# Optimization experiments

Hardware: AMD Instinct MI355X
Metric: run time of the kernel (lower is better)

Reference implementation:

```python
import jax, jax.numpy as jnp
import numpy as np

B, T, C = 4, 2048, 1024


def setup_inputs() -> dict:
    key = jax.random.key(0)
    ks = jax.random.split(key, 5)
    s = 1.0 / np.sqrt(C)
    return {
        "X": jax.random.normal(ks[0], (B, T, C), dtype=jnp.float32),
        "Wq": jax.random.normal(ks[1], (C, C), dtype=jnp.float32) * s,
        "Wk": jax.random.normal(ks[2], (C, C), dtype=jnp.float32) * s,
        "Wv": jax.random.normal(ks[3], (C, C), dtype=jnp.float32) * s,
        "Wo": jax.random.normal(ks[4], (C, C), dtype=jnp.float32) * s,
    }


def reference(X, Wq, Wk, Wv, Wo):
    Bx, Tx, Cx = X.shape
    Q = X @ Wq  # [B,T,C]
    K = X @ Wk
    V = X @ Wv
    scores = jnp.einsum('btc,bsc->bts', Q, K) / jnp.sqrt(jnp.asarray(Cx, X.dtype))
    # causal mask: position t attends to s <= t
    causal = jnp.tril(jnp.ones((Tx, Tx), dtype=bool))
    scores = jnp.where(causal, scores, jnp.asarray(-jnp.inf, scores.dtype))
    weights = jax.nn.softmax(scores, axis=-1)
    out = jnp.einsum('bts,bsc->btc', weights, V)
    return out @ Wo
```

## Files before the change

kernel.cpp:

```cpp
#include <hip/hip_runtime.h>
#include <hip/hip_bf16.h>
#include <cmath>


typedef __attribute__((ext_vector_type(8))) __bf16 bf16x8;
typedef __attribute__((ext_vector_type(8))) short short8;
typedef __attribute__((ext_vector_type(4))) float f32x4;

__device__ __forceinline__ unsigned short f2bf(float f) {
  union { float f; unsigned u; } v; v.f = f;
  unsigned u = v.u;
  u += ((u >> 16) & 1u) + 0x7fffu;
  return (unsigned short)(u >> 16);
}
__device__ __forceinline__ float bf2f(unsigned short h) {
  union { unsigned u; float f; } v; v.u = ((unsigned)h) << 16;
  return v.f;
}

#define GLDS(gp, sp)                                                           \
  __builtin_amdgcn_global_load_lds(                                            \
      (const __attribute__((address_space(1))) void*)(gp),                     \
      (__attribute__((address_space(3))) void*)(sp), 16, 0, 0)

__global__ void prep(const float* __restrict__ X,
                     const float* __restrict__ w0, const float* __restrict__ w1,
                     const float* __restrict__ w2, const float* __restrict__ w3,
                     unsigned short* __restrict__ Xb,
                     unsigned short* __restrict__ wcat,
                     unsigned short* __restrict__ wot,
                     int n) {
  if (blockIdx.z < 4) {
    const float* src = blockIdx.z == 0 ? w0 : blockIdx.z == 1 ? w1
                       : blockIdx.z == 2 ? w2 : w3;
    unsigned short* dst =
        blockIdx.z < 3 ? wcat + (size_t)blockIdx.z * n * n : wot;
    __shared__ float tile[32][33];
    int bx = blockIdx.x * 32, by = blockIdx.y * 32;
    int tx = threadIdx.x, ty = threadIdx.y;
#pragma unroll
    for (int i = 0; i < 32; i += 8)
      tile[ty + i][tx] = src[(size_t)(by + ty + i) * n + bx + tx];
    __syncthreads();
#pragma unroll
    for (int i = 0; i < 32; i += 8)
      dst[(size_t)(bx + ty + i) * n + by + tx] = f2bf(tile[tx][ty + i]);
  } else {
    const int bid = (blockIdx.z - 4) * 1024 + blockIdx.y * 32 + blockIdx.x;
    const int t = threadIdx.y * 32 + threadIdx.x;
    const int i = (bid * 256 + t) * 4;
    float4 f = *(const float4*)(X + i);
    ushort4 o = make_ushort4(f2bf(f.x), f2bf(f.y), f2bf(f.z), f2bf(f.w));
    *(ushort4*)(Xb + i) = o;
  }
}

__global__ __launch_bounds__(256, 2)
void gemm_qkv(const unsigned short* __restrict__ A, int lda,
              const unsigned short* __restrict__ B, int ldb,
              unsigned short* __restrict__ Cp, int K, int gx) {
  const int id = blockIdx.x;
  const int gs = gx * 8;
  const int g = id / gs, r = id - g * gs;
  const int bx = r >> 3;
  const int by = g * 8 + (r & 7);
  const int m0 = by * 128;
  const int n0 = bx * 128;

  const int tid  = threadIdx.x;
  const int lane = tid & 63;
  const int w    = tid >> 6;
  const int wm   = (w >> 1) * 64;
  const int wn   = (w & 1) * 64;
  const int quad = lane >> 4;
  const int l16  = lane & 15;

  __shared__ unsigned short As[8192];
  __shared__ unsigned short Bs[8192];

  f32x4 acc[4][4];
#pragma unroll
  for (int i = 0; i < 4; ++i)
#pragma unroll
    for (int j = 0; j < 4; ++j)
      acc[i][j] = (f32x4){0.f, 0.f, 0.f, 0.f};

  const int srow = tid >> 3;
  const int scol = ((tid & 7) ^ (srow & 7)) * 8;
  const unsigned short* gA = A + (long long)(m0 + srow) * lda + scol;
  const unsigned short* gB = B + (long long)(n0 + srow) * ldb + scol;
  const int rsw = l16 & 7;

  for (int kt = 0; kt < K; kt += 64) {
    __syncthreads();
#pragma unroll
    for (int r2 = 0; r2 < 4; ++r2) {
      GLDS(gA + (long long)(r2 * 32) * lda + kt, As + r2 * 2048 + tid * 8);
      GLDS(gB + (long long)(r2 * 32) * ldb + kt, Bs + r2 * 2048 + tid * 8);
    }
    __syncthreads();
#pragma unroll
    for (int ks = 0; ks < 2; ++ks) {
      bf16x8 af[4], bfr[4];
#pragma unroll
      for (int i = 0; i < 4; ++i)
        af[i] = *(const bf16x8*)(As + (wm + i * 16 + l16) * 64 +
                                 ((ks * 4 + quad) ^ rsw) * 8);
#pragma unroll
      for (int j = 0; j < 4; ++j)
        bfr[j] = *(const bf16x8*)(Bs + (wn + j * 16 + l16) * 64 +
                                  ((ks * 4 + quad) ^ rsw) * 8);
#pragma unroll
      for (int i = 0; i < 4; ++i)
#pragma unroll
        for (int j = 0; j < 4; ++j)
          acc[i][j] = __builtin_amdgcn_mfma_f32_16x16x32_bf16(af[i], bfr[j],
                                                              acc[i][j], 0, 0, 0);
    }
  }

#pragma unroll
  for (int i = 0; i < 4; ++i) {
#pragma unroll
    for (int j = 0; j < 4; ++j) {
      const int row = m0 + wm + i * 16 + quad * 4;
      const int col = n0 + wn + j * 16 + l16;
      if (col >= 2048) {
        const int b = row >> 11, t = row & 2047, cv = col - 2048;
        ushort4 o = make_ushort4(f2bf(acc[i][j][0]), f2bf(acc[i][j][1]),
                                 f2bf(acc[i][j][2]), f2bf(acc[i][j][3]));
        *(ushort4*)(Cp + 16777216LL + ((long long)(b * 1024 + cv)) * 2048 + t) = o;
      } else {
        unsigned short* dst = Cp + (col >= 1024 ? 8388608LL - 1024 : 0);
#pragma unroll
        for (int r2 = 0; r2 < 4; ++r2)
          dst[(long long)(row + r2) * 1024 + col] = f2bf(acc[i][j][r2]);
      }
    }
  }
}

template <typename OutT>
__global__ __launch_bounds__(64, 2)
void gemm64(const unsigned short* __restrict__ A, int lda, long long sA,
            const unsigned short* __restrict__ B, int ldb, long long sB,
            OutT* __restrict__ Cp, int ldc, long long sC,
            int K, float alpha, int tri, int kcap) {
  A  += (long long)blockIdx.z * sA;
  B  += (long long)blockIdx.z * sB;
  Cp += (long long)blockIdx.z * sC;

  int by, bx;
  if (tri) {
    const int idx = blockIdx.x;
    by = (int)((sqrtf(8.f * idx + 1.f) - 1.f) * 0.5f);
    while (by * (by + 1) / 2 > idx) --by;
    while ((by + 1) * (by + 2) / 2 <= idx) ++by;
    bx = idx - by * (by + 1) / 2;
  } else {
    by = blockIdx.y;
    bx = blockIdx.x;
    if (kcap) by = gridDim.y - 1 - by;
  }
  const int m0 = by * 64;
  const int n0 = bx * 64;
  const int Keff = kcap ? min(K, m0 + 64) : K;

  const int lane = threadIdx.x;
  const int quad = lane >> 4;
  const int l16  = lane & 15;
  const int rsw  = l16 & 7;

  __shared__ unsigned short As[4096];
  __shared__ unsigned short Bs[4096];

  f32x4 acc[4][4];
#pragma unroll
  for (int i = 0; i < 4; ++i)
#pragma unroll
    for (int j = 0; j < 4; ++j)
      acc[i][j] = (f32x4){0.f, 0.f, 0.f, 0.f};

  const int srow = lane >> 3;
  const int scol = ((lane & 7) ^ (srow & 7)) * 8;
  const unsigned short* gA = A + (long long)(m0 + srow) * lda + scol;
  const unsigned short* gB = B + (long long)(n0 + srow) * ldb + scol;

  for (int kt = 0; kt < Keff; kt += 64) {
    __syncthreads();
#pragma unroll
    for (int r = 0; r < 8; ++r) {
      GLDS(gA + (long long)(r * 8) * lda + kt, As + r * 512 + lane * 8);
      GLDS(gB + (long long)(r * 8) * ldb + kt, Bs + r * 512 + lane * 8);
    }
    __syncthreads();
#pragma unroll
    for (int ks = 0; ks < 2; ++ks) {
      bf16x8 af[4], bfr[4];
#pragma unroll
      for (int i = 0; i < 4; ++i)
        af[i] = *(const bf16x8*)(As + (i * 16 + l16) * 64 +
                                 ((ks * 4 + quad) ^ rsw) * 8);
#pragma unroll
      for (int j = 0; j < 4; ++j)
        bfr[j] = *(const bf16x8*)(Bs + (j * 16 + l16) * 64 +
                                  ((ks * 4 + quad) ^ rsw) * 8);
#pragma unroll
      for (int i = 0; i < 4; ++i)
#pragma unroll
        for (int j = 0; j < 4; ++j)
          acc[i][j] = __builtin_amdgcn_mfma_f32_16x16x32_bf16(af[i], bfr[j],
                                                              acc[i][j], 0, 0, 0);
    }
  }

#pragma unroll
  for (int i = 0; i < 4; ++i) {
#pragma unroll
    for (int j = 0; j < 4; ++j) {
      const int row = m0 + i * 16 + quad * 4;
      const int col = n0 + j * 16 + l16;
#pragma unroll
      for (int r = 0; r < 4; ++r) {
        float v = acc[i][j][r] * alpha;
        if constexpr (sizeof(OutT) == 2)
          Cp[(long long)(row + r) * ldc + col] = (OutT)f2bf(v);
        else
          Cp[(long long)(row + r) * ldc + col] = v;
      }
    }
  }
}

__global__ __launch_bounds__(256)
void softmax_causal(unsigned short* __restrict__ S, int T) {
  const long long row = blockIdx.x;
  const int t = (int)(row & (long long)(T - 1));
  const int limit = ((t >> 6) + 1) << 6;
  unsigned short* p = S + row * T;
  const int tid  = threadIdx.x;
  const int base = tid * 8;
  const bool active = base < limit;

  short8 raw = {};
  if (active) raw = *(const short8*)(p + base);
  float x[8];
  float mx = -1e30f;
#pragma unroll
  for (int j = 0; j < 8; ++j) {
    bool valid = active && (base + j) <= t;
    x[j] = valid ? bf2f((unsigned short)raw[j]) : -1e30f;
    mx = fmaxf(mx, x[j]);
  }
#pragma unroll
  for (int off = 32; off > 0; off >>= 1) mx = fmaxf(mx, __shfl_xor(mx, off));
  __shared__ float red[8];
  const int wv = tid >> 6;
  if ((tid & 63) == 0) red[wv] = mx;
  __syncthreads();
  mx = fmaxf(fmaxf(red[0], red[1]), fmaxf(red[2], red[3]));

  float sum = 0.f;
#pragma unroll
  for (int j = 0; j < 8; ++j) {
    bool valid = active && (base + j) <= t;
    x[j] = valid ? __expf(x[j] - mx) : 0.f;
    sum += x[j];
  }
#pragma unroll
  for (int off = 32; off > 0; off >>= 1) sum += __shfl_xor(sum, off);
  if ((tid & 63) == 0) red[4 + wv] = sum;
  __syncthreads();
  sum = red[4] + red[5] + red[6] + red[7];
  const float inv = 1.f / sum;

  if (active) {
    unsigned short out[8];
#pragma unroll
    for (int j = 0; j < 8; ++j) out[j] = f2bf(x[j] * inv);
    *(short8*)(p + base) = *(const short8*)out;
  }
}

extern "C" void kernel_launch(void* const* d_in, const int* in_sizes, int n_in,
                              void* d_out, int out_size, void* d_ws,
                              size_t ws_size, hipStream_t stream) {
  (void)in_sizes; (void)n_in; (void)out_size; (void)ws_size;
  const int Bb = 4, T = 2048, C = 1024;
  const int M = Bb * T;

  const float* X  = (const float*)d_in[0];
  const float* Wq = (const float*)d_in[1];
  const float* Wk = (const float*)d_in[2];
  const float* Wv = (const float*)d_in[3];
  const float* Wo = (const float*)d_in[4];
  float* Out = (float*)d_out;

  char* w = (char*)d_ws;
  unsigned short* Xb   = (unsigned short*)w; w += (size_t)M * C * 2;
  unsigned short* Wcat = (unsigned short*)w; w += (size_t)3 * C * C * 2;
  unsigned short* Wot  = (unsigned short*)w; w += (size_t)C * C * 2;
  unsigned short* Q    = (unsigned short*)w; w += (size_t)M * C * 2;
  unsigned short* Kb   = (unsigned short*)w; w += (size_t)M * C * 2;
  unsigned short* Vt   = (unsigned short*)w; w += (size_t)M * C * 2;
  unsigned short* O    = Xb;
  unsigned short* S    = (unsigned short*)d_out;

  prep<<<dim3(32, 32, 12), dim3(32, 8), 0, stream>>>(X, Wq, Wk, Wv, Wo, Xb,
                                                     Wcat, Wot, C);

  gemm_qkv<<<dim3((3 * C / 128) * (M / 128)), dim3(256), 0, stream>>>(
      Xb, C, Wcat, C, Q, C, 3 * C / 128);

  const int ntri = (T / 64) * (T / 64 + 1) / 2;
  gemm64<unsigned short><<<dim3(ntri, 1, Bb), dim3(64), 0, stream>>>(
      Q, C, (long long)T * C, Kb, C, (long long)T * C,
      S, T, (long long)T * T, C, 0.03125f, 1, 0);

  softmax_causal<<<M, 256, 0, stream>>>(S, T);

  gemm64<unsigned short><<<dim3(C / 64, T / 64, Bb), dim3(64), 0, stream>>>(
      S, T, (long long)T * T, Vt, T, (long long)C * T,
      O, C, (long long)T * C, T, 1.f, 0, 1);

  gemm64<float><<<dim3(C / 64, M / 64, 1), dim3(64), 0, stream>>>(
      O, C, 0, Wot, C, 0, Out, C, 0, C, 1.f, 0, 0);
}
```

Baseline: 282.2 us.

## Fold output projection into V weights and widen attention GEMM tiles to 128

Precomputes Wv·Wo as a combined weight so the V projection directly yields V·Wo, which removes the final output-projection GEMM. The P·V GEMM now writes fp32 output into a scratch buffer that is then copied to the output. The attention GEMMs move from single-wave 64x64 tiles to 128x128 tiles with 4 or 8 waves, and the softmax row limit is rounded to 128-wide blocks to match. In exchange, the folded weight product adds bf16 rounding and the change adds a device-to-device copy.

```diff
diff --git a/kernel.cpp b/kernel.cpp
--- a/kernel.cpp
+++ b/kernel.cpp
@@ -28,13 +28,21 @@
                      const float* __restrict__ w2, const float* __restrict__ w3,
                      unsigned short* __restrict__ Xb,
                      unsigned short* __restrict__ wcat,
+                     unsigned short* __restrict__ wvb,
                      unsigned short* __restrict__ wot,
                      int n) {
-  if (blockIdx.z < 4) {
-    const float* src = blockIdx.z == 0 ? w0 : blockIdx.z == 1 ? w1
-                       : blockIdx.z == 2 ? w2 : w3;
-    unsigned short* dst =
-        blockIdx.z < 3 ? wcat + (size_t)blockIdx.z * n * n : wot;
+  if (blockIdx.z == 2) {
+    int bx = blockIdx.x * 32, by = blockIdx.y * 32;
+    int tx = threadIdx.x, ty = threadIdx.y;
+#pragma unroll
+    for (int i = 0; i < 32; i += 8) {
+      size_t idx = (size_t)(by + ty + i) * n + bx + tx;
+      wvb[idx] = f2bf(w2[idx]);
+    }
+  } else if (blockIdx.z < 4) {
+    const float* src = blockIdx.z == 0 ? w0 : blockIdx.z == 1 ? w1 : w3;
+    unsigned short* dst = blockIdx.z == 0 ? wcat
+                          : blockIdx.z == 1 ? wcat + (size_t)n * n : wot;
     __shared__ float tile[32][33];
     int bx = blockIdx.x * 32, by = blockIdx.y * 32;
     int tx = threadIdx.x, ty = threadIdx.y;
@@ -52,6 +60,110 @@
     float4 f = *(const float4*)(X + i);
     ushort4 o = make_ushort4(f2bf(f.x), f2bf(f.y), f2bf(f.z), f2bf(f.w));
     *(ushort4*)(Xb + i) = o;
+  }
+}
+
+template <typename OutT, int NW>
+__global__ __launch_bounds__(NW * 64, NW / 2)
+void gemm_bt(const unsigned short* __restrict__ A, int lda, long long sA,
+             const unsigned short* __restrict__ B, int ldb, long long sB,
+             OutT* __restrict__ Cp, int ldc, long long sC,
+             int K, float alpha, int tri, int kcap, int gx) {
+  A  += (long long)blockIdx.z * sA;
+  B  += (long long)blockIdx.z * sB;
+  Cp += (long long)blockIdx.z * sC;
+
+  int by, bx;
+  if (tri) {
+    const int idx = blockIdx.x;
+    by = (int)((sqrtf(8.f * idx + 1.f) - 1.f) * 0.5f);
+    while (by * (by + 1) / 2 > idx) --by;
+    while ((by + 1) * (by + 2) / 2 <= idx) ++by;
+    bx = idx - by * (by + 1) / 2;
+  } else if (gx > 0) {
+    const int id = blockIdx.x;
+    const int gs = gx * 8;
+    const int g = id / gs, r = id - g * gs;
+    bx = r >> 3;
+    by = g * 8 + (r & 7);
+    if (kcap) by = (gridDim.x / gx) - 1 - by;
+  } else {
+    by = blockIdx.y;
+    bx = blockIdx.x;
+  }
+  const int m0 = by * 128;
+  const int n0 = bx * 128;
+  const int Keff = kcap ? min(K, m0 + 128) : K;
+
+  const int tid  = threadIdx.x;
+  const int lane = tid & 63;
+  const int w    = tid >> 6;
+  const int wm   = (NW == 4) ? (w >> 1) * 64 : (w >> 1) * 32;
+  const int wn   = (w & 1) * 64;
+  const int quad = lane >> 4;
+  const int l16  = lane & 15;
+  constexpr int AI = (NW == 4) ? 4 : 2;
+  constexpr int NR = 128 / (NW * 8);
+
+  __shared__ unsigned short As[8192];
+  __shared__ unsigned short Bs[8192];
+
+  f32x4 acc[AI][4];
+#pragma unroll
+  for (int i = 0; i < AI; ++i)
+#pragma unroll
+    for (int j = 0; j < 4; ++j)
+      acc[i][j] = (f32x4){0.f, 0.f, 0.f, 0.f};
+
+  const int srow = tid >> 3;
+  const int scol = ((tid & 7) ^ (srow & 7)) * 8;
+  const unsigned short* gA = A + (long long)(m0 + srow) * lda + scol;
+  const unsigned short* gB = B + (long long)(n0 + srow) * ldb + scol;
+  const int rsw = l16 & 7;
+
+  for (int kt = 0; kt < Keff; kt += 64) {
+    __syncthreads();
+#pragma unroll
+    for (int r = 0; r < NR; ++r) {
+      GLDS(gA + (long long)(r * NW * 8) * lda + kt, As + r * NW * 512 + tid * 8);
+      GLDS(gB + (long long)(r * NW * 8) * ldb + kt, Bs + r * NW * 512 + tid * 8);
+    }
+    __syncthreads();
+#pragma unroll
+    for (int ks = 0; ks < 2; ++ks) {
+      bf16x8 af[AI], bfr[4];
+#pragma unroll
+      for (int i = 0; i < AI; ++i)
+        af[i] = *(const bf16x8*)(As + (wm + i * 16 + l16) * 64 +
+                                 ((ks * 4 + quad) ^ rsw) * 8);
+#pragma unroll
+      for (int j = 0; j < 4; ++j)
+        bfr[j] = *(const bf16x8*)(Bs + (wn + j * 16 + l16) * 64 +
+                                  ((ks * 4 + quad) ^ rsw) * 8);
+#pragma unroll
+      for (int i = 0; i < AI; ++i)
+#pragma unroll
+        for (int j = 0; j < 4; ++j)
+          acc[i][j] = __builtin_amdgcn_mfma_f32_16x16x32_bf16(af[i], bfr[j],
+                                                              acc[i][j], 0, 0, 0);
+    }
+  }
+
+#pragma unroll
+  for (int i = 0; i < AI; ++i) {
+#pragma unroll
+    for (int j = 0; j < 4; ++j) {
+      const int row = m0 + wm + i * 16 + quad * 4;
+      const int col = n0 + wn + j * 16 + l16;
+#pragma unroll
+      for (int r = 0; r < 4; ++r) {
+        float v = acc[i][j][r] * alpha;
+        if constexpr (sizeof(OutT) == 2)
+          Cp[(long long)(row + r) * ldc + col] = (OutT)f2bf(v);
+        else
+          Cp[(long long)(row + r) * ldc + col] = v;
+      }
+    }
   }
 }
 
@@ -140,103 +252,11 @@
   }
 }
 
-template <typename OutT>
-__global__ __launch_bounds__(64, 2)
-void gemm64(const unsigned short* __restrict__ A, int lda, long long sA,
-            const unsigned short* __restrict__ B, int ldb, long long sB,
-            OutT* __restrict__ Cp, int ldc, long long sC,
-            int K, float alpha, int tri, int kcap) {
-  A  += (long long)blockIdx.z * sA;
-  B  += (long long)blockIdx.z * sB;
-  Cp += (long long)blockIdx.z * sC;
-
-  int by, bx;
-  if (tri) {
-    const int idx = blockIdx.x;
-    by = (int)((sqrtf(8.f * idx + 1.f) - 1.f) * 0.5f);
-    while (by * (by + 1) / 2 > idx) --by;
-    while ((by + 1) * (by + 2) / 2 <= idx) ++by;
-    bx = idx - by * (by + 1) / 2;
-  } else {
-    by = blockIdx.y;
-    bx = blockIdx.x;
-    if (kcap) by = gridDim.y - 1 - by;
-  }
-  const int m0 = by * 64;
-  const int n0 = bx * 64;
-  const int Keff = kcap ? min(K, m0 + 64) : K;
-
-  const int lane = threadIdx.x;
-  const int quad = lane >> 4;
-  const int l16  = lane & 15;
-  const int rsw  = l16 & 7;
-
-  __shared__ unsigned short As[4096];
-  __shared__ unsigned short Bs[4096];
-
-  f32x4 acc[4][4];
-#pragma unroll
-  for (int i = 0; i < 4; ++i)
-#pragma unroll
-    for (int j = 0; j < 4; ++j)
-      acc[i][j] = (f32x4){0.f, 0.f, 0.f, 0.f};
-
-  const int srow = lane >> 3;
-  const int scol = ((lane & 7) ^ (srow & 7)) * 8;
-  const unsigned short* gA = A + (long long)(m0 + srow) * lda + scol;
-  const unsigned short* gB = B + (long long)(n0 + srow) * ldb + scol;
-
-  for (int kt = 0; kt < Keff; kt += 64) {
-    __syncthreads();
-#pragma unroll
-    for (int r = 0; r < 8; ++r) {
-      GLDS(gA + (long long)(r * 8) * lda + kt, As + r * 512 + lane * 8);
-      GLDS(gB + (long long)(r * 8) * ldb + kt, Bs + r * 512 + lane * 8);
-    }
-    __syncthreads();
-#pragma unroll
-    for (int ks = 0; ks < 2; ++ks) {
-      bf16x8 af[4], bfr[4];
-#pragma unroll
-      for (int i = 0; i < 4; ++i)
-        af[i] = *(const bf16x8*)(As + (i * 16 + l16) * 64 +
-                                 ((ks * 4 + quad) ^ rsw) * 8);
-#pragma unroll
-      for (int j = 0; j < 4; ++j)
-        bfr[j] = *(const bf16x8*)(Bs + (j * 16 + l16) * 64 +
-                                  ((ks * 4 + quad) ^ rsw) * 8);
-#pragma unroll
-      for (int i = 0; i < 4; ++i)
-#pragma unroll
-        for (int j = 0; j < 4; ++j)
-          acc[i][j] = __builtin_amdgcn_mfma_f32_16x16x32_bf16(af[i], bfr[j],
-                                                              acc[i][j], 0, 0, 0);
-    }
-  }
-
-#pragma unroll
-  for (int i = 0; i < 4; ++i) {
-#pragma unroll
-    for (int j = 0; j < 4; ++j) {
-      const int row = m0 + i * 16 + quad * 4;
-      const int col = n0 + j * 16 + l16;
-#pragma unroll
-      for (int r = 0; r < 4; ++r) {
-        float v = acc[i][j][r] * alpha;
-        if constexpr (sizeof(OutT) == 2)
-          Cp[(long long)(row + r) * ldc + col] = (OutT)f2bf(v);
-        else
-          Cp[(long long)(row + r) * ldc + col] = v;
-      }
-    }
-  }
-}
-
 __global__ __launch_bounds__(256)
 void softmax_causal(unsigned short* __restrict__ S, int T) {
   const long long row = blockIdx.x;
   const int t = (int)(row & (long long)(T - 1));
-  const int limit = ((t >> 6) + 1) << 6;
+  const int limit = ((t >> 7) + 1) << 7;
   unsigned short* p = S + row * T;
   const int tid  = threadIdx.x;
   const int base = tid * 8;
@@ -297,32 +317,36 @@
   float* Out = (float*)d_out;
 
   char* w = (char*)d_ws;
-  unsigned short* Xb   = (unsigned short*)w; w += (size_t)M * C * 2;
   unsigned short* Wcat = (unsigned short*)w; w += (size_t)3 * C * C * 2;
-  unsigned short* Wot  = (unsigned short*)w; w += (size_t)C * C * 2;
   unsigned short* Q    = (unsigned short*)w; w += (size_t)M * C * 2;
   unsigned short* Kb   = (unsigned short*)w; w += (size_t)M * C * 2;
   unsigned short* Vt   = (unsigned short*)w; w += (size_t)M * C * 2;
-  unsigned short* O    = Xb;
+  unsigned short* Xb   = (unsigned short*)w; w += (size_t)M * C * 2;
+  unsigned short* Wvb  = (unsigned short*)d_out;
+  unsigned short* Wot  = (unsigned short*)d_out + (size_t)C * C;
   unsigned short* S    = (unsigned short*)d_out;
+  float*          OutT = (float*)Q;
 
   prep<<<dim3(32, 32, 12), dim3(32, 8), 0, stream>>>(X, Wq, Wk, Wv, Wo, Xb,
-                                                     Wcat, Wot, C);
+                                                     Wcat, Wvb, Wot, C);
+
+  gemm_bt<unsigned short, 4><<<dim3(C / 128, C / 128, 1), dim3(256), 0, stream>>>(
+      Wot, C, 0, Wvb, C, 0, Wcat + (size_t)2 * C * C, C, 0, C, 1.f, 0, 0, 0);
 
   gemm_qkv<<<dim3((3 * C / 128) * (M / 128)), dim3(256), 0, stream>>>(
       Xb, C, Wcat, C, Q, C, 3 * C / 128);
 
-  const int ntri = (T / 64) * (T / 64 + 1) / 2;
-  gemm64<unsigned short><<<dim3(ntri, 1, Bb), dim3(64), 0, stream>>>(
+  const int ntri = (T / 128) * (T / 128 + 1) / 2;
+  gemm_bt<unsigned short, 8><<<dim3(ntri, 1, Bb), dim3(512), 0, stream>>>(
       Q, C, (long long)T * C, Kb, C, (long long)T * C,
-      S, T, (long long)T * T, C, 0.03125f, 1, 0);
+      S, T, (long long)T * T, C, 0.03125f, 1, 0, 0);
 
   softmax_causal<<<M, 256, 0, stream>>>(S, T);
 
-  gemm64<unsigned short><<<dim3(C / 64, T / 64, Bb), dim3(64), 0, stream>>>(
+  gemm_bt<float, 8><<<dim3((C / 128) * (T / 128), 1, Bb), dim3(512), 0, stream>>>(
       S, T, (long long)T * T, Vt, T, (long long)C * T,
-      O, C, (long long)T * C, T, 1.f, 0, 1);
-
-  gemm64<float><<<dim3(C / 64, M / 64, 1), dim3(64), 0, stream>>>(
-      O, C, 0, Wot, C, 0, Out, C, 0, C, 1.f, 0, 0);
-}
+      OutT, C, (long long)T * C, T, 1.f, 0, 1, C / 128);
+
+  hipMemcpyAsync(Out, OutT, (size_t)M * C * sizeof(float),
+                 hipMemcpyDeviceToDevice, stream);
+}
```

Measured after the change: 267.8 us. 1.05x faster.
